# Kernel optimization log

Measured on AMD Instinct MI355X. Metric: run time of the kernel, lower is better.

Reference implementation:

```python
import jax, jax.numpy as jnp
import numpy as np

B, S, D, H = 4, 2048, 1024, 16
HD = D // H
SCALE = np.sqrt(HD).astype(np.float32)


def setup_inputs() -> dict:
    key = jax.random.key(0)
    ks = jax.random.split(key, 6)
    std = 1.0 / np.sqrt(D)
    return {
        "query": jax.random.normal(ks[0], (B, S, D), jnp.float32),
        "key": jax.random.normal(ks[1], (B, S, D), jnp.float32),
        "value": jax.random.normal(ks[2], (B, S, D), jnp.float32),
        "Wq": jax.random.normal(ks[3], (D, D), jnp.float32) * std,
        "bq": jnp.zeros((D,), jnp.float32),
        "Wk": jax.random.normal(ks[4], (D, D), jnp.float32) * std,
        "bk": jnp.zeros((D,), jnp.float32),
        "Wv": jax.random.normal(ks[5], (D, D), jnp.float32) * std,
        "bv": jnp.zeros((D,), jnp.float32),
    }


def _split_heads(x):
    # [B,S,D] -> [B,H,S,HD]
    return x.reshape(B, S, H, HD).transpose(0, 2, 1, 3)


def reference(query, key, value, Wq, bq, Wk, bk, Wv, bv):
    q = _split_heads(query @ Wq.T + bq)
    k = _split_heads(key @ Wk.T + bk)
    v = _split_heads(value @ Wv.T + bv)
    scores = jnp.einsum("bhqd,bhkd->bhqk", q, k) / SCALE
    attn = jax.nn.softmax(scores, axis=-1)  # dropout=0 (eval)
    ctx = jnp.einsum("bhqk,bhkd->bhqd", attn, v)
    return ctx.transpose(0, 2, 1, 3).reshape(B, S, D)
```

## Files before the change

kernel.cpp:

```cpp
#include <hip/hip_runtime.h>
#include <hip/hip_bf16.h>

typedef __attribute__((ext_vector_type(8))) short bf16x8;
typedef __attribute__((ext_vector_type(4))) float f32x4;
typedef __attribute__((ext_vector_type(16))) float f32x16;

#define SEQ 2048
#define DMODEL 1024
#define NH 16
#define HD 64
#define BATCH 4
#define BHTOT 64
#define BS 8192
#define QKV_ELEMS 8388608

#define C2EXP 0.1803368801111244f

__device__ __forceinline__ ushort f2bf(float f) {
  union { float f; unsigned u; } v; v.f = f;
  unsigned r = (v.u + 0x7FFFu + ((v.u >> 16) & 1u)) >> 16;
  return (ushort)r;
}

__device__ __forceinline__ unsigned pkbf(float a, float b) {
  union { __hip_bfloat162 h; unsigned u; } cv;
  cv.h = __float22bfloat162_rn(make_float2(a, b));
  return cv.u;
}

#if __has_builtin(__builtin_amdgcn_exp2f)
#define EXP2F(x) __builtin_amdgcn_exp2f(x)
#else
#define EXP2F(x) exp2f(x)
#endif

#define GLD16(gp, lp)                                                        \
  __builtin_amdgcn_global_load_lds(                                          \
      (const __attribute__((address_space(1))) void*)(gp),                   \
      (__attribute__((address_space(3))) void*)(lp), 16, 0, 0)

__global__ __launch_bounds__(256) void convert_all(
    const float* __restrict__ x0, const float* __restrict__ x1,
    const float* __restrict__ x2,
    const float* __restrict__ w0, const float* __restrict__ w1,
    const float* __restrict__ w2,
    ushort* __restrict__ xout, ushort* __restrict__ wout) {
  const int zz = blockIdx.y;
  const float* src;
  ushort* dst;
  size_t e;
  if (blockIdx.x < 8192) {
    src = zz == 0 ? x0 : (zz == 1 ? x1 : x2);
    dst = xout + (size_t)zz * QKV_ELEMS;
    e = ((size_t)blockIdx.x * 256 + threadIdx.x) * 4;
  } else {
    src = zz == 0 ? w0 : (zz == 1 ? w1 : w2);
    dst = wout + (size_t)zz * 1048576;
    e = ((size_t)(blockIdx.x - 8192) * 256 + threadIdx.x) * 4;
  }
  float4 v = *(const float4*)(src + e);
  ushort4 o = { f2bf(v.x), f2bf(v.y), f2bf(v.z), f2bf(v.w) };
  *(ushort4*)(dst + e) = o;
}

__global__ __launch_bounds__(256) void convert_w(
    const float* __restrict__ w0, const float* __restrict__ w1,
    const float* __restrict__ w2, ushort* __restrict__ out) {
  const float* src = blockIdx.y == 0 ? w0 : (blockIdx.y == 1 ? w1 : w2);
  size_t e = ((size_t)blockIdx.x * 256 + threadIdx.x) * 4;
  float4 v = *(const float4*)(src + e);
  ushort4 o = { f2bf(v.x), f2bf(v.y), f2bf(v.z), f2bf(v.w) };
  *(ushort4*)(out + (size_t)blockIdx.y * 1048576 + e) = o;
}

__global__ __launch_bounds__(256) void qkv_gemm_bf(
    const ushort* __restrict__ Xb, const ushort* __restrict__ Wb,
    const float* __restrict__ bq, const float* __restrict__ bk, const float* __restrict__ bv,
    ushort* __restrict__ qkv) {
  __shared__ ushort sA[128][32];
  __shared__ ushort sB[128][32];

  const int z = blockIdx.z;
  const int rbid = blockIdx.y * 64 + blockIdx.x;
  const int bid = (rbid & 7) * 64 + (rbid >> 3);
  const int bx = bid & 63, by = bid >> 6;

  const ushort* A = Xb + (size_t)z * QKV_ELEMS;
  const ushort* W = Wb + (size_t)z * 1048576;
  const float* bias = z == 0 ? bq : (z == 1 ? bk : bv);
  const float oscale = z == 0 ? C2EXP : 1.0f;
  ushort* out = qkv + (size_t)z * QKV_ELEMS;

  const int t = threadIdx.x;
  const int m0 = bx * 128;
  const int n0 = by * 128;
  const int w = t >> 6, l = t & 63, lr = l & 15, lhi = l >> 4;
  const int wr = (w >> 1) * 64, wc = (w & 1) * 64;

  const int rl = l >> 2;
  const int scol = ((l & 3) * 8) ^ ((rl & 3) << 3);
  const int rcol = (lhi * 8) ^ ((lr & 3) << 3);

  f32x4 acc[4][4];
#pragma unroll
  for (int i = 0; i < 4; i++)
#pragma unroll
    for (int j = 0; j < 4; j++) acc[i][j] = (f32x4){0.f, 0.f, 0.f, 0.f};

  for (int k0 = 0; k0 < DMODEL; k0 += 32) {
#pragma unroll
    for (int i = 0; i < 2; i++) {
      int c = w * 2 + i;
      GLD16(A + (size_t)(m0 + c * 16 + rl) * DMODEL + k0 + scol, &sA[c * 16][0]);
      GLD16(W + (size_t)(n0 + c * 16 + rl) * DMODEL + k0 + scol, &sB[c * 16][0]);
    }
    __syncthreads();
    bf16x8 af[4], bfr[4];
#pragma unroll
    for (int mi = 0; mi < 4; mi++) af[mi] = *(const bf16x8*)(&sA[wr + mi * 16 + lr][rcol]);
#pragma unroll
    for (int ni = 0; ni < 4; ni++) bfr[ni] = *(const bf16x8*)(&sB[wc + ni * 16 + lr][rcol]);
#pragma unroll
    for (int mi = 0; mi < 4; mi++)
#pragma unroll
      for (int ni = 0; ni < 4; ni++)
        acc[mi][ni] = __builtin_amdgcn_mfma_f32_16x16x32_bf16(af[mi], bfr[ni], acc[mi][ni], 0, 0, 0);
    __syncthreads();
  }

#pragma unroll
  for (int mi = 0; mi < 4; mi++) {
#pragma unroll
    for (int ni = 0; ni < 4; ni++) {
      int col = n0 + wc + ni * 16 + lr;
      float bsv = bias[col];
      int h = col >> 6, hd = col & 63;
#pragma unroll
      for (int r = 0; r < 4; r++) {
        int row = m0 + wr + mi * 16 + lhi * 4 + r;
        int b = row >> 11, s = row & 2047;
        float vv = (acc[mi][ni][r] + bsv) * oscale;
        out[(((size_t)(b * NH + h)) * SEQ + s) * HD + hd] = f2bf(vv);
      }
    }
  }
}

__global__ __launch_bounds__(256) void qkv_gemm_f32(
    const float* __restrict__ x0, const float* __restrict__ x1, const float* __restrict__ x2,
    const ushort* __restrict__ Wb,
    const float* __restrict__ bq, const float* __restrict__ bk, const float* __restrict__ bv,
    ushort* __restrict__ qkv) {
  __shared__ ushort sA[128][40];
  __shared__ ushort sB[128][40];

  const int z = blockIdx.z;
  const float* X = z == 0 ? x0 : (z == 1 ? x1 : x2);
  const ushort* W = Wb + (size_t)z * 1048576;
  const float* bias = z == 0 ? bq : (z == 1 ? bk : bv);
  const float oscale = z == 0 ? C2EXP : 1.0f;
  ushort* out = qkv + (size_t)z * QKV_ELEMS;

  const int t = threadIdx.x;
  const int m0 = blockIdx.x * 128;
  const int n0 = blockIdx.y * 128;
  const int w = t >> 6, l = t & 63, lr = l & 15, lhi = l >> 4;
  const int wr = (w >> 1) * 64, wc = (w & 1) * 64;

  f32x4 acc[4][4];
#pragma unroll
  for (int i = 0; i < 4; i++)
#pragma unroll
    for (int j = 0; j < 4; j++) acc[i][j] = (f32x4){0.f, 0.f, 0.f, 0.f};

  for (int k0 = 0; k0 < DMODEL; k0 += 32) {
#pragma unroll
    for (int i = 0; i < 4; i++) {
      int e = i * 256 + t;
      int row = e >> 3, col = (e & 7) * 4;
      float4 a = *(const float4*)(X + (size_t)(m0 + row) * DMODEL + k0 + col);
      ushort4 ab = { f2bf(a.x), f2bf(a.y), f2bf(a.z), f2bf(a.w) };
      *(ushort4*)(&sA[row][col]) = ab;
      ushort4 bb = *(const ushort4*)(W + (size_t)(n0 + row) * DMODEL + k0 + col);
      *(ushort4*)(&sB[row][col]) = bb;
    }
    __syncthreads();
    bf16x8 af[4], bfr[4];
#pragma unroll
    for (int mi = 0; mi < 4; mi++) af[mi] = *(const bf16x8*)(&sA[wr + mi * 16 + lr][lhi * 8]);
#pragma unroll
    for (int ni = 0; ni < 4; ni++) bfr[ni] = *(const bf16x8*)(&sB[wc + ni * 16 + lr][lhi * 8]);
#pragma unroll
    for (int mi = 0; mi < 4; mi++)
#pragma unroll
      for (int ni = 0; ni < 4; ni++)
        acc[mi][ni] = __builtin_amdgcn_mfma_f32_16x16x32_bf16(af[mi], bfr[ni], acc[mi][ni], 0, 0, 0);
    __syncthreads();
  }

#pragma unroll
  for (int mi = 0; mi < 4; mi++) {
#pragma unroll
    for (int ni = 0; ni < 4; ni++) {
      int col = n0 + wc + ni * 16 + lr;
      float bsv = bias[col];
      int h = col >> 6, hd = col & 63;
#pragma unroll
      for (int r = 0; r < 4; r++) {
        int row = m0 + wr + mi * 16 + lhi * 4 + r;
        int b = row >> 11, s = row & 2047;
        float vv = (acc[mi][ni][r] + bsv) * oscale;
        out[(((size_t)(b * NH + h)) * SEQ + s) * HD + hd] = f2bf(vv);
      }
    }
  }
}

__global__ __launch_bounds__(256) void transpose_v(const ushort* __restrict__ vsrc,
                                                   ushort* __restrict__ vtg) {
  __shared__ ushort T[64][72];
  const int s0 = blockIdx.x * 64;
  const int bh = blockIdx.y;
  const int t = threadIdx.x;
  const int r = t >> 2, c16 = (t & 3) * 16;

  const ushort* src = vsrc + ((size_t)bh * SEQ + s0 + r) * HD + c16;
  uint4 a = *(const uint4*)(src);
  uint4 b = *(const uint4*)(src + 8);
  *(uint4*)(&T[r][c16]) = a;
  *(uint4*)(&T[r][c16 + 8]) = b;
  __syncthreads();

  ushort o[16];
#pragma unroll
  for (int jj = 0; jj < 16; jj++) {
    int sj = (jj & 3) | ((jj & 4) << 1) | ((jj & 8) >> 1);
    o[jj] = T[c16 + sj][r];
  }
  ushort* dst = vtg + ((size_t)bh * HD + r) * SEQ + s0 + c16;
  *(uint4*)(dst) = *(uint4*)(&o[0]);
  *(uint4*)(dst + 8) = *(uint4*)(&o[8]);
}

__global__ __launch_bounds__(256, 4) void attn_kernel(const ushort* __restrict__ qkv,
                                                      const ushort* __restrict__ vtg,
                                                      float* __restrict__ out) {
  __shared__ ushort Kt[2][64][72];
  __shared__ ushort Vt[2][64][72];

  const int rb = blockIdx.x;
  const int bid = (rb & 7) * 128 + (rb >> 3);
  const int bh = bid >> 4, qt = bid & 15;
  const int q0 = qt * 128;
  const int t = threadIdx.x, w = t >> 6, l = t & 63;
  const int lq = l & 31, hi = l >> 5, hi8 = hi * 8;

  const ushort* q = qkv;
  const size_t base = (size_t)bh * SEQ * HD;
  const ushort* kb = qkv + QKV_ELEMS + base;
  const ushort* vb = vtg + (size_t)bh * HD * SEQ;

  const int rr = t >> 3, kcol = (t & 7) * 8;

  bf16x8 aq[4];
  {
    int qrow = q0 + w * 32 + lq;
#pragma unroll
    for (int ks = 0; ks < 4; ks++)
      aq[ks] = *(const bf16x8*)(q + base + (size_t)qrow * HD + ks * 16 + hi8);
  }

  float lsum = 0.f;
  f32x16 acc_o[2];
  acc_o[0] = (f32x16)(0.0f);
  acc_o[1] = (f32x16)(0.0f);

#pragma unroll
  for (int i = 0; i < 2; i++) {
    bf16x8 g0 = *(const bf16x8*)(kb + (size_t)(i * 32 + rr) * HD + kcol);
    *(bf16x8*)(&Kt[0][i * 32 + rr][kcol]) = g0;
    bf16x8 g1 = *(const bf16x8*)(vb + (size_t)(i * 32 + rr) * SEQ + kcol);
    *(bf16x8*)(&Vt[0][i * 32 + rr][kcol]) = g1;
  }
  __syncthreads();

  for (int tile = 0; tile < SEQ / 64; tile++) {
    const int cur = tile & 1, nxt = cur ^ 1;
    const int kvn = ((tile + 1) & 31) * 64;

    bf16x8 gk[2], gv[2];
#pragma unroll
    for (int i = 0; i < 2; i++) {
      gk[i] = *(const bf16x8*)(kb + (size_t)(kvn + i * 32 + rr) * HD + kcol);
      gv[i] = *(const bf16x8*)(vb + (size_t)(i * 32 + rr) * SEQ + kvn + kcol);
    }

#pragma unroll
    for (int mt = 0; mt < 2; mt++) {
      f32x16 sc = (f32x16)(0.0f);
#pragma unroll
      for (int ks = 0; ks < 4; ks++) {
        bf16x8 ak = *(const bf16x8*)(&Kt[cur][mt * 32 + lq][ks * 16 + hi8]);
        sc = __builtin_amdgcn_mfma_f32_32x32x16_bf16(ak, aq[ks], sc, 0, 0, 0);
      }

#pragma unroll
      for (int sp = 0; sp < 2; sp++) {
        const int e0 = sp * 8;
        union { unsigned u[4]; bf16x8 v8; } ap;
#pragma unroll
        for (int j = 0; j < 4; j++) {
          float p0 = EXP2F(sc[e0 + 2 * j]);
          float p1 = EXP2F(sc[e0 + 2 * j + 1]);
          lsum += p0 + p1;
          ap.u[j] = pkbf(p0, p1);
        }
        const int s = mt * 2 + sp;
#pragma unroll
        for (int nt = 0; nt < 2; nt++) {
          bf16x8 bv = *(const bf16x8*)(&Vt[cur][nt * 32 + lq][s * 16 + hi8]);
          acc_o[nt] = __builtin_amdgcn_mfma_f32_32x32x16_bf16(ap.v8, bv, acc_o[nt], 0, 0, 0);
        }
      }
    }

#pragma unroll
    for (int i = 0; i < 2; i++) {
      *(bf16x8*)(&Kt[nxt][i * 32 + rr][kcol]) = gk[i];
      *(bf16x8*)(&Vt[nxt][i * 32 + rr][kcol]) = gv[i];
    }
    __syncthreads();
  }

  lsum += __shfl_xor(lsum, 32);
  const int b = bh >> 4, h = bh & 15;
  float inv = 1.f / lsum;
#pragma unroll
  for (int r = 0; r < 16; r++) {
    int rowq = (r & 3) + 8 * (r >> 2) + 4 * hi;
    float iv = __shfl(inv, (l & 32) | rowq);
    int s = q0 + w * 32 + rowq;
#pragma unroll
    for (int nt = 0; nt < 2; nt++)
      out[((size_t)(b * SEQ + s)) * DMODEL + h * HD + nt * 32 + lq] = acc_o[nt][r] * iv;
  }
}

extern "C" void kernel_launch(void* const* d_in, const int* in_sizes, int n_in,
                              void* d_out, int out_size, void* d_ws, size_t ws_size,
                              hipStream_t stream) {
  const float* query = (const float*)d_in[0];
  const float* key_  = (const float*)d_in[1];
  const float* value = (const float*)d_in[2];
  const float* Wq = (const float*)d_in[3];
  const float* bq = (const float*)d_in[4];
  const float* Wk = (const float*)d_in[5];
  const float* bk = (const float*)d_in[6];
  const float* Wv = (const float*)d_in[7];
  const float* bv = (const float*)d_in[8];

  ushort* Wb = (ushort*)d_ws;
  ushort* qkv = Wb + 3u * 1048576u;
  ushort* Xb = qkv + 3u * (size_t)QKV_ELEMS;
  ushort* Vtg = Xb;
  const size_t need_bf = (3u * 1048576u + 6u * (size_t)QKV_ELEMS) * 2u;

  if (ws_size >= need_bf) {
    convert_all<<<dim3(8192 + 1024, 3), 256, 0, stream>>>(query, key_, value,
                                                          Wq, Wk, Wv, Xb, Wb);
    qkv_gemm_bf<<<dim3(64, 8, 3), 256, 0, stream>>>(Xb, Wb, bq, bk, bv, qkv);
  } else {
    convert_w<<<dim3(1024, 3), 256, 0, stream>>>(Wq, Wk, Wv, Wb);
    qkv_gemm_f32<<<dim3(64, 8, 3), 256, 0, stream>>>(query, key_, value, Wb, bq, bk, bv, qkv);
  }
  transpose_v<<<dim3(SEQ / 64, BHTOT), 256, 0, stream>>>(qkv + 2u * (size_t)QKV_ELEMS, Vtg);
  attn_kernel<<<dim3(BHTOT * (SEQ / 128)), 256, 0, stream>>>(qkv, Vtg, (float*)d_out);
}
```

Baseline: 199.9 us.

## Fuse V transpose into QKV GEMM epilogue via shared-memory staging

For the V projection, the bf16 GEMM epilogue now stages the output tile in shared memory, transposed, and writes V directly in [bh][hd][seq] layout with vectorized 16-byte stores. This removes the separate transpose_v launch and its extra read/write pass over V on the workspace path. The block-index swizzle for L2 locality is also dropped in favor of direct blockIdx mapping. The epilogue gains extra syncs and shared-memory traffic, and Q/K blocks keep the scattered scalar stores.

```diff
diff --git a/kernel.cpp b/kernel.cpp
--- a/kernel.cpp
+++ b/kernel.cpp
@@ -77,14 +77,11 @@
     const ushort* __restrict__ Xb, const ushort* __restrict__ Wb,
     const float* __restrict__ bq, const float* __restrict__ bk, const float* __restrict__ bv,
     ushort* __restrict__ qkv) {
-  __shared__ ushort sA[128][32];
-  __shared__ ushort sB[128][32];
+  __shared__ ushort smem[8704];
+  ushort (*sA)[32] = (ushort(*)[32])smem;
+  ushort (*sB)[32] = (ushort(*)[32])(smem + 4096);
 
   const int z = blockIdx.z;
-  const int rbid = blockIdx.y * 64 + blockIdx.x;
-  const int bid = (rbid & 7) * 64 + (rbid >> 3);
-  const int bx = bid & 63, by = bid >> 6;
-
   const ushort* A = Xb + (size_t)z * QKV_ELEMS;
   const ushort* W = Wb + (size_t)z * 1048576;
   const float* bias = z == 0 ? bq : (z == 1 ? bk : bv);
@@ -92,8 +89,8 @@
   ushort* out = qkv + (size_t)z * QKV_ELEMS;
 
   const int t = threadIdx.x;
-  const int m0 = bx * 128;
-  const int n0 = by * 128;
+  const int m0 = blockIdx.x * 128;
+  const int n0 = blockIdx.y * 128;
   const int w = t >> 6, l = t & 63, lr = l & 15, lhi = l >> 4;
   const int wr = (w >> 1) * 64, wc = (w & 1) * 64;
 
@@ -128,19 +125,48 @@
     __syncthreads();
   }
 
-#pragma unroll
-  for (int mi = 0; mi < 4; mi++) {
-#pragma unroll
-    for (int ni = 0; ni < 4; ni++) {
-      int col = n0 + wc + ni * 16 + lr;
-      float bsv = bias[col];
-      int h = col >> 6, hd = col & 63;
-#pragma unroll
-      for (int r = 0; r < 4; r++) {
-        int row = m0 + wr + mi * 16 + lhi * 4 + r;
-        int b = row >> 11, s = row & 2047;
-        float vv = (acc[mi][ni][r] + bsv) * oscale;
-        out[(((size_t)(b * NH + h)) * SEQ + s) * HD + hd] = f2bf(vv);
+  if (z == 2) {
+    ushort (*T)[136] = (ushort(*)[136])smem;
+    const int lhip = ((lhi & 1) << 1) | (lhi >> 1);
+    const int b = m0 >> 11;
+#pragma unroll
+    for (int chalf = 0; chalf < 2; ++chalf) {
+      __syncthreads();
+      if (wc == chalf * 64) {
+#pragma unroll
+        for (int ni = 0; ni < 4; ni++) {
+          int col = n0 + wc + ni * 16 + lr;
+          float bsv = bias[col];
+#pragma unroll
+          for (int mi = 0; mi < 4; mi++)
+#pragma unroll
+            for (int r = 0; r < 4; r++)
+              T[ni * 16 + lr][wr + mi * 16 + lhip * 4 + r] = f2bf(acc[mi][ni][r] + bsv);
+        }
+      }
+      __syncthreads();
+      const int c2 = t >> 2, so = (t & 3) * 32;
+      const int bh = b * NH + ((n0 + chalf * 64) >> 6);
+      ushort* dst = out + ((size_t)bh * HD + c2) * SEQ + (m0 & 2047) + so;
+#pragma unroll
+      for (int j = 0; j < 4; j++)
+        *(uint4*)(dst + j * 8) = *(const uint4*)(&T[c2][so + j * 8]);
+    }
+  } else {
+#pragma unroll
+    for (int mi = 0; mi < 4; mi++) {
+#pragma unroll
+      for (int ni = 0; ni < 4; ni++) {
+        int col = n0 + wc + ni * 16 + lr;
+        float bsv = bias[col];
+        int h = col >> 6, hd = col & 63;
+#pragma unroll
+        for (int r = 0; r < 4; r++) {
+          int row = m0 + wr + mi * 16 + lhi * 4 + r;
+          int b = row >> 11, s = row & 2047;
+          float vv = (acc[mi][ni][r] + bsv) * oscale;
+          out[(((size_t)(b * NH + h)) * SEQ + s) * HD + hd] = f2bf(vv);
+        }
       }
     }
   }
@@ -362,17 +388,18 @@
   ushort* Wb = (ushort*)d_ws;
   ushort* qkv = Wb + 3u * 1048576u;
   ushort* Xb = qkv + 3u * (size_t)QKV_ELEMS;
-  ushort* Vtg = Xb;
   const size_t need_bf = (3u * 1048576u + 6u * (size_t)QKV_ELEMS) * 2u;
 
   if (ws_size >= need_bf) {
     convert_all<<<dim3(8192 + 1024, 3), 256, 0, stream>>>(query, key_, value,
                                                           Wq, Wk, Wv, Xb, Wb);
     qkv_gemm_bf<<<dim3(64, 8, 3), 256, 0, stream>>>(Xb, Wb, bq, bk, bv, qkv);
+    attn_kernel<<<dim3(BHTOT * (SEQ / 128)), 256, 0, stream>>>(
+        qkv, qkv + 2u * (size_t)QKV_ELEMS, (float*)d_out);
   } else {
     convert_w<<<dim3(1024, 3), 256, 0, stream>>>(Wq, Wk, Wv, Wb);
     qkv_gemm_f32<<<dim3(64, 8, 3), 256, 0, stream>>>(query, key_, value, Wb, bq, bk, bv, qkv);
-  }
-  transpose_v<<<dim3(SEQ / 64, BHTOT), 256, 0, stream>>>(qkv + 2u * (size_t)QKV_ELEMS, Vtg);
-  attn_kernel<<<dim3(BHTOT * (SEQ / 128)), 256, 0, stream>>>(qkv, Vtg, (float*)d_out);
-}
+    transpose_v<<<dim3(SEQ / 64, BHTOT), 256, 0, stream>>>(qkv + 2u * (size_t)QKV_ELEMS, Xb);
+    attn_kernel<<<dim3(BHTOT * (SEQ / 128)), 256, 0, stream>>>(qkv, Xb, (float*)d_out);
+  }
+}
```

After: 194.7 us. 1.03x faster.
